# Optimization experiments

Measured on AMD Instinct MI355X. Metric: run time of the kernel, lower is better.

## Reference

```python
import jax, jax.numpy as jnp
import numpy as np

N, M, D = 1024, 1024, 256

def setup_inputs() -> dict:
    key = jax.random.key(0)
    ks = jax.random.split(key, 10)
    s = 1.0 / np.sqrt(D)
    return {
        "f_r": jax.random.normal(ks[0], (N, D), jnp.float32),
        "f_r_prime": jax.random.normal(ks[1], (M, D), jnp.float32),
        "W_w": jax.random.uniform(ks[2], (D, D), jnp.float32, -s, s),
        "W_b": jax.random.uniform(ks[3], (D,), jnp.float32, -s, s),
        "Wp_w": jax.random.uniform(ks[4], (D, D), jnp.float32, -s, s),
        "Wp_b": jax.random.uniform(ks[5], (D,), jnp.float32, -s, s),
        "w_w": jax.random.uniform(ks[6], (1, D), jnp.float32, -s, s),
        "w_b": jax.random.uniform(ks[7], (1,), jnp.float32, -s, s),
        "wp_w": jax.random.uniform(ks[8], (1, D), jnp.float32, -s, s),
        "wp_b": jax.random.uniform(ks[9], (1,), jnp.float32, -s, s),
    }

def reference(f_r, f_r_prime, W_w, W_b, Wp_w, Wp_b, w_w, w_b, wp_w, wp_b):
    q = f_r @ W_w.T + W_b            # [N, D]
    k = f_r_prime @ Wp_w.T + Wp_b    # [M, D]
    # additive (Bahdanau) scores: tanh over broadcast sum [N, M, D]
    h = jnp.tanh(q[:, None, :] + k[None, :, :])
    alpha = h @ w_w.T + w_b          # [N, M, 1]
    alpha = jax.nn.softmax(alpha, axis=1)
    # stage-1 pooling over M (weights on raw f_r_prime, as in source)
    context = jnp.sum(alpha * f_r_prime[None, :, :], axis=1)  # [N, D]
    # stage-2 attention pooling over N
    alpha_p = jax.nn.softmax(context @ wp_w.T + wp_b, axis=0)  # [N, 1]
    pool = jnp.sum(alpha_p * context, axis=0, keepdims=True)   # [1, D]
    return pool
```

## Files before the change

### kernel.cpp

```cpp
#include <hip/hip_runtime.h>

#define NN 1024
#define MM 1024
#define DD 256

typedef float floatx2 __attribute__((ext_vector_type(2)));

__device__ __forceinline__ float rcp_fast(float x) { return __builtin_amdgcn_rcpf(x); }

__global__ __launch_bounds__(256) void gemm_exp_kernel(
    const float* __restrict__ f_r,  const float* __restrict__ W_w,  const float* __restrict__ W_b,
    const float* __restrict__ f_rp, const float* __restrict__ Wp_w, const float* __restrict__ Wp_b,
    float* __restrict__ Eq, float* __restrict__ EkT, float* __restrict__ out0)
{
    __shared__ float As[32][36];
    __shared__ float Bs[32][68];
    __shared__ float T[64][36];

    const int b = blockIdx.x;
    const int t = threadIdx.x;
    if (b == 0) out0[t] = 0.f;

    const int mat  = b >> 7;
    const int tile = b & 127;
    const int rt = tile & 31, dt = tile >> 5;
    const float* __restrict__ A    = mat ? f_rp : f_r;
    const float* __restrict__ B    = mat ? Wp_w : W_w;
    const float* __restrict__ bias = mat ? Wp_b : W_b;

    const int tx = t & 15, ty = t >> 4;
    const int r0 = rt * 32, d0 = dt * 64;
    const int ar = t >> 3, ak = (t & 7) * 4;
    const int br = t >> 2, bk = (t & 3) * 8;

    float acc[2][4];
    #pragma unroll
    for (int i = 0; i < 2; ++i)
        #pragma unroll
        for (int j = 0; j < 4; ++j) acc[i][j] = 0.f;

    for (int kk = 0; kk < DD; kk += 32) {
        float4 av  = *(const float4*)(A + (size_t)(r0 + ar) * DD + kk + ak);
        float4 bv0 = *(const float4*)(B + (size_t)(d0 + br) * DD + kk + bk);
        float4 bv1 = *(const float4*)(B + (size_t)(d0 + br) * DD + kk + bk + 4);
        __syncthreads();
        As[ak + 0][ar] = av.x; As[ak + 1][ar] = av.y; As[ak + 2][ar] = av.z; As[ak + 3][ar] = av.w;
        Bs[bk + 0][br] = bv0.x; Bs[bk + 1][br] = bv0.y; Bs[bk + 2][br] = bv0.z; Bs[bk + 3][br] = bv0.w;
        Bs[bk + 4][br] = bv1.x; Bs[bk + 5][br] = bv1.y; Bs[bk + 6][br] = bv1.z; Bs[bk + 7][br] = bv1.w;
        __syncthreads();
        #pragma unroll
        for (int k = 0; k < 32; ++k) {
            float2 a2 = *(const float2*)&As[k][ty * 2];
            float4 b4 = *(const float4*)&Bs[k][tx * 4];
            float aa[2] = {a2.x, a2.y};
            float bb[4] = {b4.x, b4.y, b4.z, b4.w};
            #pragma unroll
            for (int i = 0; i < 2; ++i)
                #pragma unroll
                for (int j = 0; j < 4; ++j)
                    acc[i][j] = fmaf(aa[i], bb[j], acc[i][j]);
        }
    }

    float bj[4];
    #pragma unroll
    for (int j = 0; j < 4; ++j) bj[j] = bias[d0 + tx * 4 + j];

    float e[2][4];
    #pragma unroll
    for (int i = 0; i < 2; ++i)
        #pragma unroll
        for (int j = 0; j < 4; ++j) {
            float v = acc[i][j] + bj[j];
            v = fminf(fmaxf(v, -5.f), 5.f);
            e[i][j] = __expf(2.f * v);
        }

    if (mat == 0) {
        #pragma unroll
        for (int i = 0; i < 2; ++i)
            *(float4*)&Eq[(size_t)(r0 + ty * 2 + i) * DD + d0 + tx * 4] =
                make_float4(e[i][0], e[i][1], e[i][2], e[i][3]);
    } else {
        __syncthreads();
        #pragma unroll
        for (int i = 0; i < 2; ++i)
            #pragma unroll
            for (int j = 0; j < 4; ++j) T[tx * 4 + j][ty * 2 + i] = e[i][j];
        __syncthreads();
        const int dl = t >> 3, rl = (t & 7) * 4;
        #pragma unroll
        for (int h = 0; h < 2; ++h) {
            int dloc = dl + 32 * h;
            float4 tv = *(const float4*)&T[dloc][rl];
            *(float4*)&EkT[(size_t)(d0 + dloc) * MM + r0 + rl] = tv;
        }
    }
}

__global__ __launch_bounds__(1024, 4) void fused_attn_kernel(
    const float* __restrict__ Eq, const float* __restrict__ EkT,
    const float* __restrict__ w_w, const float* __restrict__ frp,
    const float* __restrict__ wp_w,
    float* __restrict__ ctx, float* __restrict__ score)
{
    __shared__ float accbuf[4][16][256];
    __shared__ float alsm[4][MM];
    __shared__ float4 ctxred[16][4][64];
    __shared__ float redmx[4][4];
    __shared__ float redsm[4][4];
    __shared__ float redsc[16];

    const int t  = threadIdx.x;
    const int tg = t >> 8;
    const int tm = t & 255;
    const int n0 = blockIdx.x * 4;

    const int dh = __builtin_amdgcn_readfirstlane(tg * 64);
    const float* __restrict__ eqb = Eq + (size_t)n0 * DD + dh;
    const float* __restrict__ wwb = w_w + dh;

    const floatx2 one2 = {1.f, 1.f};
    floatx2 accl[4] = {{0.f,0.f},{0.f,0.f},{0.f,0.f},{0.f,0.f}};
    floatx2 acch[4] = {{0.f,0.f},{0.f,0.f},{0.f,0.f},{0.f,0.f}};

    const float* ekb = EkT + (size_t)dh * MM + 4 * tm;
    float4 c0 = *(const float4*)(ekb + 0 * MM);
    float4 c1 = *(const float4*)(ekb + 1 * MM);
    float4 c2 = *(const float4*)(ekb + 2 * MM);
    float4 c3 = *(const float4*)(ekb + 3 * MM);

    for (int gi = 0; gi < 16; ++gi) {
        float4 p0 = c0, p1 = c1, p2 = c2, p3 = c3;
        if (gi < 15) {
            const float* nb = ekb + (size_t)(gi * 4 + 4) * MM;
            p0 = *(const float4*)(nb + 0 * MM);
            p1 = *(const float4*)(nb + 1 * MM);
            p2 = *(const float4*)(nb + 2 * MM);
            p3 = *(const float4*)(nb + 3 * MM);
        }
        const int db = gi * 4;
        float4 w4 = *(const float4*)(wwb + db);
        floatx2 kv[4][2] = {{{c0.x, c0.y}, {c0.z, c0.w}},
                            {{c1.x, c1.y}, {c1.z, c1.w}},
                            {{c2.x, c2.y}, {c2.z, c2.w}},
                            {{c3.x, c3.y}, {c3.z, c3.w}}};
        #pragma unroll
        for (int n = 0; n < 4; ++n) {
            float4 q4 = *(const float4*)(eqb + n * DD + db);
            #pragma unroll
            for (int h = 0; h < 2; ++h) {
                floatx2 x0 = q4.x * kv[0][h] + one2;
                floatx2 x1 = q4.y * kv[1][h] + one2;
                floatx2 x2 = q4.z * kv[2][h] + one2;
                floatx2 x3 = q4.w * kv[3][h] + one2;
                floatx2 p01 = x0 * x1;
                floatx2 p23 = x2 * x3;
                floatx2 n01 = w4.x * x1 + w4.y * x0;
                floatx2 n23 = w4.z * x3 + w4.w * x2;
                floatx2 nc  = n01 * p23 + n23 * p01;
                floatx2 pt  = p01 * p23;
                floatx2 r;  r.x = rcp_fast(pt.x);  r.y = rcp_fast(pt.y);
                if (h == 0) accl[n] += nc * r; else acch[n] += nc * r;
            }
        }
        c0 = p0; c1 = p1; c2 = p2; c3 = p3;
    }

    float acc[4][4];
    #pragma unroll
    for (int n = 0; n < 4; ++n) {
        acc[n][0] = -2.f * accl[n].x; acc[n][1] = -2.f * accl[n].y;
        acc[n][2] = -2.f * acch[n].x; acc[n][3] = -2.f * acch[n].y;
    }

    #pragma unroll
    for (int n = 0; n < 4; ++n)
        #pragma unroll
        for (int j = 0; j < 4; ++j) accbuf[tg][n * 4 + j][tm] = acc[n][j];
    __syncthreads();

    const int g = tg;
    const int w4id = (t >> 6) & 3;
    const int lane = t & 63;
    float aj[4];
    #pragma unroll
    for (int j = 0; j < 4; ++j)
        aj[j] = accbuf[0][g * 4 + j][tm] + accbuf[1][g * 4 + j][tm]
              + accbuf[2][g * 4 + j][tm] + accbuf[3][g * 4 + j][tm];

    float mx = fmaxf(fmaxf(aj[0], aj[1]), fmaxf(aj[2], aj[3]));
    #pragma unroll
    for (int off = 32; off > 0; off >>= 1) mx = fmaxf(mx, __shfl_xor(mx, off));
    if (lane == 0) redmx[g][w4id] = mx;
    __syncthreads();
    const float MX = fmaxf(fmaxf(redmx[g][0], redmx[g][1]), fmaxf(redmx[g][2], redmx[g][3]));

    float e[4], sm = 0.f;
    #pragma unroll
    for (int j = 0; j < 4; ++j) { e[j] = __expf(aj[j] - MX); sm += e[j]; }
    #pragma unroll
    for (int off = 32; off > 0; off >>= 1) sm += __shfl_xor(sm, off);
    if (lane == 0) redsm[g][w4id] = sm;
    __syncthreads();
    const float S = redsm[g][0] + redsm[g][1] + redsm[g][2] + redsm[g][3];
    const float inv = rcp_fast(S);
    *(float4*)&alsm[g][4 * tm] = make_float4(e[0] * inv, e[1] * inv, e[2] * inv, e[3] * inv);
    __syncthreads();

    const int cc = t & 63;
    const int rr = t >> 6;
    const int m0 = rr * 64;
    floatx2 axl[4] = {{0.f,0.f},{0.f,0.f},{0.f,0.f},{0.f,0.f}};
    floatx2 axh[4] = {{0.f,0.f},{0.f,0.f},{0.f,0.f},{0.f,0.f}};
    const float* fb = frp + (size_t)m0 * DD + 4 * cc;
    for (int m4 = 0; m4 < 16; ++m4) {
        float alv[4][4];
        #pragma unroll
        for (int n = 0; n < 4; ++n) {
            float4 a4 = *(const float4*)&alsm[n][m0 + m4 * 4];
            alv[n][0] = a4.x; alv[n][1] = a4.y; alv[n][2] = a4.z; alv[n][3] = a4.w;
        }
        #pragma unroll
        for (int mm = 0; mm < 4; ++mm) {
            float4 f = *(const float4*)(fb + (size_t)(m4 * 4 + mm) * DD);
            floatx2 fl = {f.x, f.y}, fh = {f.z, f.w};
            #pragma unroll
            for (int n = 0; n < 4; ++n) {
                axl[n] += alv[n][mm] * fl;
                axh[n] += alv[n][mm] * fh;
            }
        }
    }
    #pragma unroll
    for (int n = 0; n < 4; ++n)
        ctxred[rr][n][cc] = make_float4(axl[n].x, axl[n].y, axh[n].x, axh[n].y);
    __syncthreads();

    const int nn = t >> 8, d = t & 255;
    float s = 0.f;
    #pragma unroll
    for (int r = 0; r < 16; ++r)
        s += ((const float*)&ctxred[r][nn][d >> 2])[d & 3];
    ctx[(size_t)(n0 + nn) * DD + d] = s;

    float p = s * wp_w[d];
    #pragma unroll
    for (int off = 32; off > 0; off >>= 1) p += __shfl_xor(p, off);
    if (lane == 0) redsc[t >> 6] = p;
    __syncthreads();
    if (t < 4) score[n0 + t] = redsc[4 * t] + redsc[4 * t + 1] + redsc[4 * t + 2] + redsc[4 * t + 3];
}

__global__ __launch_bounds__(256) void pool_kernel(
    const float* __restrict__ ctx, const float* __restrict__ score,
    float* __restrict__ out)
{
    __shared__ float red[8];
    const int t = threadIdx.x, lane = t & 63, wid = t >> 6;
    const int n0 = blockIdx.x * 4;

    float s0 = score[t], s1 = score[t + 256], s2 = score[t + 512], s3 = score[t + 768];
    float mx = fmaxf(fmaxf(s0, s1), fmaxf(s2, s3));
    #pragma unroll
    for (int off = 32; off > 0; off >>= 1) mx = fmaxf(mx, __shfl_xor(mx, off));
    if (lane == 0) red[wid] = mx;
    __syncthreads();
    mx = fmaxf(fmaxf(red[0], red[1]), fmaxf(red[2], red[3]));

    float se = __expf(s0 - mx) + __expf(s1 - mx) + __expf(s2 - mx) + __expf(s3 - mx);
    #pragma unroll
    for (int off = 32; off > 0; off >>= 1) se += __shfl_xor(se, off);
    if (lane == 0) red[4 + wid] = se;
    __syncthreads();
    se = red[4] + red[5] + red[6] + red[7];
    float invS = rcp_fast(se);

    float r = 0.f;
    #pragma unroll
    for (int i = 0; i < 4; ++i) {
        float ap = __expf(score[n0 + i] - mx) * invS;
        r = fmaf(ap, ctx[(size_t)(n0 + i) * DD + t], r);
    }
    atomicAdd(out + t, r);
}

extern "C" void kernel_launch(void* const* d_in, const int* in_sizes, int n_in,
                              void* d_out, int out_size, void* d_ws, size_t ws_size,
                              hipStream_t stream) {
    const float* f_r  = (const float*)d_in[0];
    const float* f_rp = (const float*)d_in[1];
    const float* W_w  = (const float*)d_in[2];
    const float* W_b  = (const float*)d_in[3];
    const float* Wp_w = (const float*)d_in[4];
    const float* Wp_b = (const float*)d_in[5];
    const float* w_w  = (const float*)d_in[6];
    const float* wp_w = (const float*)d_in[8];
    float* out = (float*)d_out;

    float* ws    = (float*)d_ws;
    float* Eq    = ws;
    float* EkT   = ws + 262144;
    float* ctx   = ws + 524288;
    float* score = ws + 786432;

    gemm_exp_kernel<<<256, 256, 0, stream>>>(f_r, W_w, W_b, f_rp, Wp_w, Wp_b, Eq, EkT, out);
    fused_attn_kernel<<<256, 1024, 0, stream>>>(Eq, EkT, w_w, f_rp, wp_w, ctx, score);
    pool_kernel<<<256, 256, 0, stream>>>(ctx, score, out);
}
```

Measured before the change: 122.8 us.

## Shrink shared memory and prefetch q/w to raise fused attention occupancy

Raises the launch bound's min-blocks hint from 4 to 8 and merges the two large shared buffers into one union array. Each thread group now keeps its own partial sums in registers, so only the other three partials go through shared memory. The context reduction is rebuilt with 8 row groups of 128 columns using float2 loads instead of 16 groups of 64 with float4 loads. The q and w_w loads are software-prefetched one step ahead like the k loads. Together these aim to fit more blocks per CU and hide load latency, at the risk of register spills under the tighter register budget.

```diff
diff --git a/kernel.cpp b/kernel.cpp
--- a/kernel.cpp
+++ b/kernel.cpp
@@ -98,15 +98,14 @@
     }
 }
 
-__global__ __launch_bounds__(1024, 4) void fused_attn_kernel(
+__global__ __launch_bounds__(1024, 8) void fused_attn_kernel(
     const float* __restrict__ Eq, const float* __restrict__ EkT,
     const float* __restrict__ w_w, const float* __restrict__ frp,
     const float* __restrict__ wp_w,
     float* __restrict__ ctx, float* __restrict__ score)
 {
-    __shared__ float accbuf[4][16][256];
+    __shared__ float uni[12288];
     __shared__ float alsm[4][MM];
-    __shared__ float4 ctxred[16][4][64];
     __shared__ float redmx[4][4];
     __shared__ float redsm[4][4];
     __shared__ float redsc[16];
@@ -130,41 +129,55 @@
     float4 c2 = *(const float4*)(ekb + 2 * MM);
     float4 c3 = *(const float4*)(ekb + 3 * MM);
 
+    float4 wc = *(const float4*)(wwb);
+    float4 qc[4];
+    #pragma unroll
+    for (int n = 0; n < 4; ++n) qc[n] = *(const float4*)(eqb + n * DD);
+
     for (int gi = 0; gi < 16; ++gi) {
         float4 p0 = c0, p1 = c1, p2 = c2, p3 = c3;
+        float4 wn = wc, qn[4];
+        #pragma unroll
+        for (int n = 0; n < 4; ++n) qn[n] = qc[n];
         if (gi < 15) {
-            const float* nb = ekb + (size_t)(gi * 4 + 4) * MM;
+            const int dn = gi * 4 + 4;
+            const float* nb = ekb + (size_t)dn * MM;
             p0 = *(const float4*)(nb + 0 * MM);
             p1 = *(const float4*)(nb + 1 * MM);
             p2 = *(const float4*)(nb + 2 * MM);
             p3 = *(const float4*)(nb + 3 * MM);
-        }
-        const int db = gi * 4;
-        float4 w4 = *(const float4*)(wwb + db);
-        floatx2 kv[4][2] = {{{c0.x, c0.y}, {c0.z, c0.w}},
-                            {{c1.x, c1.y}, {c1.z, c1.w}},
-                            {{c2.x, c2.y}, {c2.z, c2.w}},
-                            {{c3.x, c3.y}, {c3.z, c3.w}}};
+            wn = *(const float4*)(wwb + dn);
+            #pragma unroll
+            for (int n = 0; n < 4; ++n) qn[n] = *(const float4*)(eqb + n * DD + dn);
+        }
+        floatx2 k0l = {c0.x, c0.y}, k0h = {c0.z, c0.w};
+        floatx2 k1l = {c1.x, c1.y}, k1h = {c1.z, c1.w};
+        floatx2 k2l = {c2.x, c2.y}, k2h = {c2.z, c2.w};
+        floatx2 k3l = {c3.x, c3.y}, k3h = {c3.z, c3.w};
+        const float4 w4 = wc;
         #pragma unroll
         for (int n = 0; n < 4; ++n) {
-            float4 q4 = *(const float4*)(eqb + n * DD + db);
+            const float4 q4 = qc[n];
             #pragma unroll
             for (int h = 0; h < 2; ++h) {
-                floatx2 x0 = q4.x * kv[0][h] + one2;
-                floatx2 x1 = q4.y * kv[1][h] + one2;
-                floatx2 x2 = q4.z * kv[2][h] + one2;
-                floatx2 x3 = q4.w * kv[3][h] + one2;
+                floatx2 x0 = q4.x * (h ? k0h : k0l) + one2;
+                floatx2 x1 = q4.y * (h ? k1h : k1l) + one2;
+                floatx2 x2 = q4.z * (h ? k2h : k2l) + one2;
+                floatx2 x3 = q4.w * (h ? k3h : k3l) + one2;
                 floatx2 p01 = x0 * x1;
                 floatx2 p23 = x2 * x3;
                 floatx2 n01 = w4.x * x1 + w4.y * x0;
                 floatx2 n23 = w4.z * x3 + w4.w * x2;
                 floatx2 nc  = n01 * p23 + n23 * p01;
                 floatx2 pt  = p01 * p23;
-                floatx2 r;  r.x = rcp_fast(pt.x);  r.y = rcp_fast(pt.y);
-                if (h == 0) accl[n] += nc * r; else acch[n] += nc * r;
+                floatx2 r2;  r2.x = rcp_fast(pt.x);  r2.y = rcp_fast(pt.y);
+                if (h == 0) accl[n] += nc * r2; else acch[n] += nc * r2;
             }
         }
         c0 = p0; c1 = p1; c2 = p2; c3 = p3;
+        wc = wn;
+        #pragma unroll
+        for (int n = 0; n < 4; ++n) qc[n] = qn[n];
     }
 
     float acc[4][4];
@@ -175,9 +188,13 @@
     }
 
     #pragma unroll
-    for (int n = 0; n < 4; ++n)
-        #pragma unroll
-        for (int j = 0; j < 4; ++j) accbuf[tg][n * 4 + j][tm] = acc[n][j];
+    for (int n = 0; n < 4; ++n) {
+        if (n == tg) continue;
+        const int c = (tg < n) ? tg : tg - 1;
+        #pragma unroll
+        for (int j = 0; j < 4; ++j)
+            uni[((n * 4 + j) * 3 + c) * 256 + tm] = acc[n][j];
+    }
     __syncthreads();
 
     const int g = tg;
@@ -186,8 +203,10 @@
     float aj[4];
     #pragma unroll
     for (int j = 0; j < 4; ++j)
-        aj[j] = accbuf[0][g * 4 + j][tm] + accbuf[1][g * 4 + j][tm]
-              + accbuf[2][g * 4 + j][tm] + accbuf[3][g * 4 + j][tm];
+        aj[j] = acc[g][j]
+              + uni[((g * 4 + j) * 3 + 0) * 256 + tm]
+              + uni[((g * 4 + j) * 3 + 1) * 256 + tm]
+              + uni[((g * 4 + j) * 3 + 2) * 256 + tm];
 
     float mx = fmaxf(fmaxf(aj[0], aj[1]), fmaxf(aj[2], aj[3]));
     #pragma unroll
@@ -208,13 +227,12 @@
     *(float4*)&alsm[g][4 * tm] = make_float4(e[0] * inv, e[1] * inv, e[2] * inv, e[3] * inv);
     __syncthreads();
 
-    const int cc = t & 63;
-    const int rr = t >> 6;
-    const int m0 = rr * 64;
-    floatx2 axl[4] = {{0.f,0.f},{0.f,0.f},{0.f,0.f},{0.f,0.f}};
-    floatx2 axh[4] = {{0.f,0.f},{0.f,0.f},{0.f,0.f},{0.f,0.f}};
-    const float* fb = frp + (size_t)m0 * DD + 4 * cc;
-    for (int m4 = 0; m4 < 16; ++m4) {
+    const int cc = t & 127;
+    const int rr = t >> 7;
+    const int m0 = rr * 128;
+    floatx2 ax[4] = {{0.f,0.f},{0.f,0.f},{0.f,0.f},{0.f,0.f}};
+    const float* fb = frp + (size_t)m0 * DD + 2 * cc;
+    for (int m4 = 0; m4 < 32; ++m4) {
         float alv[4][4];
         #pragma unroll
         for (int n = 0; n < 4; ++n) {
@@ -223,25 +241,24 @@
         }
         #pragma unroll
         for (int mm = 0; mm < 4; ++mm) {
-            float4 f = *(const float4*)(fb + (size_t)(m4 * 4 + mm) * DD);
-            floatx2 fl = {f.x, f.y}, fh = {f.z, f.w};
-            #pragma unroll
-            for (int n = 0; n < 4; ++n) {
-                axl[n] += alv[n][mm] * fl;
-                axh[n] += alv[n][mm] * fh;
-            }
-        }
-    }
-    #pragma unroll
-    for (int n = 0; n < 4; ++n)
-        ctxred[rr][n][cc] = make_float4(axl[n].x, axl[n].y, axh[n].x, axh[n].y);
+            float2 f = *(const float2*)(fb + (size_t)(m4 * 4 + mm) * DD);
+            floatx2 fv = {f.x, f.y};
+            #pragma unroll
+            for (int n = 0; n < 4; ++n) ax[n] += alv[n][mm] * fv;
+        }
+    }
+    #pragma unroll
+    for (int n = 0; n < 4; ++n) {
+        float2* row = (float2*)&uni[(rr * 4 + n) * 256];
+        row[cc] = make_float2(ax[n].x, ax[n].y);
+    }
     __syncthreads();
 
     const int nn = t >> 8, d = t & 255;
     float s = 0.f;
     #pragma unroll
-    for (int r = 0; r < 16; ++r)
-        s += ((const float*)&ctxred[r][nn][d >> 2])[d & 3];
+    for (int r = 0; r < 8; ++r)
+        s += uni[(r * 4 + nn) * 256 + d];
     ctx[(size_t)(n0 + nn) * DD + d] = s;
 
     float p = s * wp_w[d];
```

After: 231.1 us. +88.2%, slower.
